# Optimization experiments

Hardware: AMD Instinct MI355X
Metric: run time of the kernel (lower is better)

Reference implementation:

```python
import jax, jax.numpy as jnp
import numpy as np

HEAD_DIM = 128
NUM_QUERY_GROUPS = 4
BLOCK_SIZE = 64
NUM_SELECTED = 16


def setup_inputs() -> dict:
    key = jax.random.key(0)
    k1, k2, k3, k4 = jax.random.split(key, 4)
    query = jax.random.normal(k1, (4, 32, 1, 128), jnp.float32)
    compressed_keys = jax.random.normal(k2, (4, 32, 128, 128), jnp.float32)
    keys = jax.random.normal(k3, (4, 4, 8192, 128), jnp.float32)
    values = jax.random.normal(k4, (4, 4, 8192, 128), jnp.float32)
    return {"query": query, "compressed_keys": compressed_keys, "keys": keys, "values": values}


def reference(query, compressed_keys, keys, values):
    # --- compressed attention importance scores ---
    q = query[:, :, -1, :]                                     # [B, H, D] (last query position)
    scale = 1.0 / (HEAD_DIM ** 0.5)
    scores = jnp.einsum('bhd,bhnd->bhn', q, compressed_keys) * scale  # [B, H, N]
    probs = jax.nn.softmax(scores, axis=-1)
    # --- GQA pooling: mean over heads within each query group ---
    B, H, N = probs.shape
    probs = probs.reshape(B, NUM_QUERY_GROUPS, H // NUM_QUERY_GROUPS, N).mean(axis=2)  # [B, G, N]
    # --- top-k block selection ---
    _, idx = jax.lax.top_k(probs, NUM_SELECTED)                # [B, G, n]
    block_starts = idx * BLOCK_SIZE                            # [B, G, n]
    offsets = jnp.arange(BLOCK_SIZE, dtype=block_starts.dtype)
    gather_idx = (block_starts[..., None] + offsets).reshape(B, NUM_QUERY_GROUPS, NUM_SELECTED * BLOCK_SIZE)  # [B, G, n*bs]
    # --- gather whole K/V blocks ---
    selected_keys = jnp.take_along_axis(keys, gather_idx[..., None], axis=2)    # [B, G, n*bs, D]
    selected_values = jnp.take_along_axis(values, gather_idx[..., None], axis=2)
    return selected_keys, selected_values
```

## Files before the change

### kernel.cpp

```cpp
#include <hip/hip_runtime.h>
#include <math.h>

#define BB   4
#define HH   32
#define GG   4
#define HPG  8
#define DD   128
#define NCK  128
#define SEQ  8192
#define NSEL 16
#define BLK  64

__global__ __launch_bounds__(512, 1) void gemv_kernel(const float* __restrict__ query,
                                                      const float* __restrict__ ck,
                                                      float* __restrict__ scores_out) {
    const int blk  = blockIdx.x;
    const int bh   = blk >> 1;
    const int half = blk & 1;
    const int t    = threadIdx.x;
    const int r    = (t >> 3) + half * 64;
    const int sub  = t & 7;

    __shared__ float q_sh[DD];
    if (t < DD) q_sh[t] = query[(size_t)bh * DD + t];
    __syncthreads();

    const float4* c4 = (const float4*)(ck + ((size_t)bh * NCK + r) * DD) + sub;
    const float4* q4 = ((const float4*)q_sh) + sub;
    float s = 0.0f;
    #pragma unroll
    for (int i = 0; i < 4; ++i) {
        float4 a = q4[i * 8];
        float4 c = c4[i * 8];
        s += a.x * c.x + a.y * c.y + a.z * c.z + a.w * c.w;
    }
    s += __shfl_xor(s, 1);
    s += __shfl_xor(s, 2);
    s += __shfl_xor(s, 4);

    if (sub == 0) scores_out[(size_t)bh * NCK + r] = s * 0.08838834764831845f;
}

__global__ __launch_bounds__(256, 1) void select_gather_kernel(const float* __restrict__ scores,
                                                               const float* __restrict__ keys,
                                                               const float* __restrict__ values,
                                                               float* __restrict__ out) {
    const int bid  = blockIdx.x;
    const int q2   = bid & 3;
    const int isV  = q2 >> 1;
    const int half = q2 & 1;
    const int s    = (bid >> 2) & 15;
    const int bg   = bid >> 6;
    const int b    = bg >> 2;
    const int g    = bg & 3;
    const int t    = threadIdx.x;
    const int w    = t >> 6;

    __shared__ float reds[2][HPG];
    __shared__ float pm[NCK];
    __shared__ int   sel_sh;

    float e[HPG];

    if (t < NCK) {
        #pragma unroll
        for (int j = 0; j < HPG; ++j)
            e[j] = expf(scores[(size_t)(b * HH + g * HPG + j) * NCK + t]);
        #pragma unroll
        for (int j = 0; j < HPG; ++j) {
            float ssum = e[j];
            #pragma unroll
            for (int off = 1; off < 64; off <<= 1) ssum += __shfl_xor(ssum, off);
            if ((t & 63) == 0) reds[w][j] = ssum;
        }
    }
    __syncthreads();

    if (t < NCK) {
        float p = 0.0f;
        #pragma unroll
        for (int j = 0; j < HPG; ++j) p += e[j] / (reds[0][j] + reds[1][j]);
        pm[t] = p;
    }
    __syncthreads();

    if (t < NCK) {
        const float mv = pm[t];
        int rank = 0;
        for (int i = 0; i < NCK; ++i) {
            const float vi = pm[i];
            if (vi > mv || (vi == mv && i < t)) ++rank;
        }
        if (rank == s) sel_sh = t;
    }
    __syncthreads();
    const int sel = sel_sh;

    const size_t src  = ((size_t)bg * SEQ + (size_t)sel * BLK + half * 32) * DD;
    const size_t dst  = ((size_t)bg * (NSEL * BLK) + (size_t)s * BLK + half * 32) * DD;
    const size_t VOFF = (size_t)BB * GG * NSEL * BLK * DD;

    const float4* sp = (const float4*)((isV ? values : keys) + src);
    float4*       dp = (float4*)(out + (isV ? VOFF : 0) + dst);

    #pragma unroll
    for (int i = 0; i < 4; ++i) dp[i * 256 + t] = sp[i * 256 + t];
}

extern "C" void kernel_launch(void* const* d_in, const int* in_sizes, int n_in,
                              void* d_out, int out_size, void* d_ws, size_t ws_size,
                              hipStream_t stream) {
    const float* query  = (const float*)d_in[0];
    const float* ck     = (const float*)d_in[1];
    const float* keys   = (const float*)d_in[2];
    const float* values = (const float*)d_in[3];
    float* out = (float*)d_out;

    float* scores = (float*)d_ws;

    gemv_kernel<<<BB * HH * 2, 512, 0, stream>>>(query, ck, scores);
    select_gather_kernel<<<BB * GG * NSEL * 4, 256, 0, stream>>>(scores, keys, values, out);
}
```

Baseline: 20.13 us.

## Fuse score GEMV and select-gather into one cooperative kernel with grid sync

Replaces the two kernel launches with a single cooperative launch of 1024 blocks. Each block first computes 16 compressed-key scores, then all blocks wait at a grid-wide sync before doing softmax, top-k ranking and the block gather. This removes the second launch and the gap between kernels, at the cost of a grid barrier and the requirement that all 1024 blocks be resident at once.

```diff
diff --git a/kernel.cpp b/kernel.cpp
--- a/kernel.cpp
+++ b/kernel.cpp
@@ -1,5 +1,8 @@
 #include <hip/hip_runtime.h>
+#include <hip/hip_cooperative_groups.h>
 #include <math.h>
+
+namespace cg = cooperative_groups;
 
 #define BB   4
 #define HH   32
@@ -11,41 +14,49 @@
 #define NSEL 16
 #define BLK  64
 
-__global__ __launch_bounds__(512, 1) void gemv_kernel(const float* __restrict__ query,
-                                                      const float* __restrict__ ck,
-                                                      float* __restrict__ scores_out) {
-    const int blk  = blockIdx.x;
-    const int bh   = blk >> 1;
-    const int half = blk & 1;
-    const int t    = threadIdx.x;
-    const int r    = (t >> 3) + half * 64;
-    const int sub  = t & 7;
+__global__ __launch_bounds__(256, 4) void fused_coop_kernel(
+    const float* __restrict__ query,
+    const float* __restrict__ ck,
+    const float* __restrict__ keys,
+    const float* __restrict__ values,
+    float* __restrict__ scores,
+    float* __restrict__ out)
+{
+    const int bid = blockIdx.x;
+    const int t   = threadIdx.x;
 
     __shared__ float q_sh[DD];
-    if (t < DD) q_sh[t] = query[(size_t)bh * DD + t];
-    __syncthreads();
+    __shared__ float reds[2][HPG];
+    __shared__ float pm[NCK];
+    __shared__ int   sel_sh;
 
-    const float4* c4 = (const float4*)(ck + ((size_t)bh * NCK + r) * DD) + sub;
-    const float4* q4 = ((const float4*)q_sh) + sub;
-    float s = 0.0f;
-    #pragma unroll
-    for (int i = 0; i < 4; ++i) {
-        float4 a = q4[i * 8];
-        float4 c = c4[i * 8];
-        s += a.x * c.x + a.y * c.y + a.z * c.z + a.w * c.w;
+    {
+        const int bh   = bid >> 3;
+        const int r    = (bid & 7) * 16 + (t >> 4);
+        const int lane = t & 15;
+
+        if (t < DD) q_sh[t] = query[(size_t)bh * DD + t];
+        __syncthreads();
+
+        const float4* c4 = (const float4*)(ck + ((size_t)bh * NCK + r) * DD) + lane;
+        const float4* q4 = ((const float4*)q_sh) + lane;
+        float s = 0.0f;
+        #pragma unroll
+        for (int i = 0; i < 2; ++i) {
+            float4 a = q4[i * 16];
+            float4 c = c4[i * 16];
+            s += a.x * c.x + a.y * c.y + a.z * c.z + a.w * c.w;
+        }
+        s += __shfl_xor(s, 1);
+        s += __shfl_xor(s, 2);
+        s += __shfl_xor(s, 4);
+        s += __shfl_xor(s, 8);
+
+        if (lane == 0) scores[(size_t)bh * NCK + r] = s * 0.08838834764831845f;
     }
-    s += __shfl_xor(s, 1);
-    s += __shfl_xor(s, 2);
-    s += __shfl_xor(s, 4);
 
-    if (sub == 0) scores_out[(size_t)bh * NCK + r] = s * 0.08838834764831845f;
-}
+    cg::this_grid().sync();
 
-__global__ __launch_bounds__(256, 1) void select_gather_kernel(const float* __restrict__ scores,
-                                                               const float* __restrict__ keys,
-                                                               const float* __restrict__ values,
-                                                               float* __restrict__ out) {
-    const int bid  = blockIdx.x;
     const int q2   = bid & 3;
     const int isV  = q2 >> 1;
     const int half = q2 & 1;
@@ -53,12 +64,7 @@
     const int bg   = bid >> 6;
     const int b    = bg >> 2;
     const int g    = bg & 3;
-    const int t    = threadIdx.x;
     const int w    = t >> 6;
-
-    __shared__ float reds[2][HPG];
-    __shared__ float pm[NCK];
-    __shared__ int   sel_sh;
 
     float e[HPG];
 
@@ -114,10 +120,12 @@
     const float* ck     = (const float*)d_in[1];
     const float* keys   = (const float*)d_in[2];
     const float* values = (const float*)d_in[3];
-    float* out = (float*)d_out;
-
+    float* out    = (float*)d_out;
     float* scores = (float*)d_ws;
 
-    gemv_kernel<<<BB * HH * 2, 512, 0, stream>>>(query, ck, scores);
-    select_gather_kernel<<<BB * GG * NSEL * 4, 256, 0, stream>>>(scores, keys, values, out);
+    void* args[] = { (void*)&query, (void*)&ck, (void*)&keys, (void*)&values,
+                     (void*)&scores, (void*)&out };
+    hipLaunchCooperativeKernel((const void*)fused_coop_kernel,
+                               dim3(BB * GG * NSEL * 4), dim3(256),
+                               args, 0, stream);
 }
```

Measured after the change: 74.75 us. 3.71x slower.
